# Performance work log

Hardware: AMD Instinct MI355X
Metric: run time of the kernel (lower is better)

## Reference

```python
import jax, jax.numpy as jnp
import numpy as np

E, HID, T, B, NH, DFF, A, C = 116, 64, 512, 64, 4, 2048, 116, 90


def _ln(x, g, b, eps=1e-5):
    m = x.mean(-1, keepdims=True)
    v = ((x - m) ** 2).mean(-1, keepdims=True)
    return (x - m) / jnp.sqrt(v + eps) * g + b


def _layer(x, p):
    # torch TransformerEncoderLayer, post-norm, relu, eval mode (no dropout)
    wqkv, bqkv, wo, bo, g1, bn1, w1, b1, w2, b2, g2, bn2 = p
    S, N, Em = x.shape  # note: S is the attended axis (dim 0), N the batched axis
    dh = Em // NH
    qkv = x @ wqkv.T + bqkv
    q, k, v = jnp.split(qkv, 3, axis=-1)
    q = q.reshape(S, N, NH, dh)
    k = k.reshape(S, N, NH, dh)
    v = v.reshape(S, N, NH, dh)
    scores = jnp.einsum('snhd,tnhd->nhst', q, k) / np.float32(np.sqrt(dh))
    attn = jax.nn.softmax(scores, axis=-1)
    o = jnp.einsum('nhst,tnhd->snhd', attn, v).reshape(S, N, Em)
    o = o @ wo.T + bo
    x = _ln(x + o, g1, bn1)
    f = jax.nn.relu(x @ w1.T + b1) @ w2.T + b2
    return _ln(x + f, g2, bn2)


def _forward(x, sim, p1, p2, fc_w, fc_b):
    out = _layer(x, p1)
    out1 = _layer(out, p2)
    outs = jnp.transpose(out1, (0, 2, 1))       # (B, E, T)
    fea_ = outs @ fc_w.T + fc_b                 # (B, E, HID)
    feas = jnp.transpose(fea_, (0, 2, 1))       # (B, HID, E)
    fea = feas[:, None, :, :, None]             # (B,1,HID,E,1)
    sim32 = sim.astype(jnp.float32)             # (A, HID, C)
    # cosine_similarity over the HID axis (dim=2 of broadcast tensors),
    # computed without materializing the (B,A,HID,E,C) broadcast product.
    dot = jnp.einsum('bhd,ahc->badc', feas, sim32)           # (B,A,E,C)
    fn = jnp.linalg.norm(feas, axis=1)                       # (B,E)
    sn = jnp.linalg.norm(sim32, axis=1)                      # (A,C)
    denom = jnp.maximum(fn[:, None, :, None] * sn[None, :, None, :], 1e-8)
    similarity = dot / denom                                 # (B,A,E,C)
    similar = similarity.reshape(-1, 116 * 90)
    nrm = jnp.maximum(jnp.linalg.norm(similar, axis=1, keepdims=True), 1e-12)
    similar = similar / nrm
    return fea, similarity, similar


_PNAMES = ['wqkv', 'bqkv', 'wo', 'bo', 'g1', 'bn1', 'w1', 'b1', 'w2', 'b2', 'g2', 'bn2']
_PSHAPES = [(3 * E, E), (3 * E,), (E, E), (E,), (E,), (E,), (DFF, E), (DFF,), (E, DFF), (E,), (E,), (E,)]


def setup_inputs() -> dict:
    key = jax.random.key(0)
    ks = jax.random.split(key, 32)
    s = 0.02
    inp = {
        'x': jax.random.normal(ks[0], (B, T, E), jnp.float32),
        'sim': jax.random.normal(ks[1], (A, HID, C), jnp.float32),
    }
    i = 2
    for L in ('l1', 'l2'):
        for nm, sh in zip(_PNAMES, _PSHAPES):
            if nm in ('g1', 'g2'):
                inp[f'{L}_{nm}'] = jnp.ones(sh, jnp.float32)
            elif nm in ('bqkv', 'bo', 'bn1', 'b1', 'b2', 'bn2'):
                inp[f'{L}_{nm}'] = jnp.zeros(sh, jnp.float32)
            else:
                inp[f'{L}_{nm}'] = jax.random.normal(ks[i], sh, jnp.float32) * s
                i += 1
    inp['fc_w'] = jax.random.normal(ks[i], (HID, T), jnp.float32) * s
    inp['fc_b'] = jnp.zeros((HID,), jnp.float32)
    return inp


def reference(x, sim,
              l1_wqkv, l1_bqkv, l1_wo, l1_bo, l1_g1, l1_bn1, l1_w1, l1_b1, l1_w2, l1_b2, l1_g2, l1_bn2,
              l2_wqkv, l2_bqkv, l2_wo, l2_bo, l2_g1, l2_bn1, l2_w1, l2_b1, l2_w2, l2_b2, l2_g2, l2_bn2,
              fc_w, fc_b):
    p1 = (l1_wqkv, l1_bqkv, l1_wo, l1_bo, l1_g1, l1_bn1, l1_w1, l1_b1, l1_w2, l1_b2, l1_g2, l1_bn2)
    p2 = (l2_wqkv, l2_bqkv, l2_wo, l2_bo, l2_g1, l2_bn1, l2_w1, l2_b1, l2_w2, l2_b2, l2_g2, l2_bn2)
    return _forward(x, sim, p1, p2, fc_w, fc_b)
```

## Files before the change

kernel.cpp:

```cpp
#include <hip/hip_runtime.h>
#include <hip/hip_bf16.h>

typedef __attribute__((ext_vector_type(8))) short short8v;
typedef __attribute__((ext_vector_type(4))) float floatx4;

__device__ __forceinline__ float bf2f(unsigned short u) {
  union { unsigned int i; float f; } c;
  c.i = ((unsigned int)u) << 16;
  return c.f;
}
__device__ __forceinline__ unsigned short f2bf(float f) {
  __hip_bfloat16 h = __float2bfloat16(f);
  return *reinterpret_cast<unsigned short*>(&h);
}

struct ConvJobs {
  const float* src[9];
  unsigned short* dst[9];
  int K[9];
  int Kp[9];
  int mode[9];
  int cum[10];
};

__global__ __launch_bounds__(256) void convert_all_kernel(ConvJobs J) {
  const int total = J.cum[9];
  for (int idx = blockIdx.x * 256 + threadIdx.x; idx < total;
       idx += gridDim.x * 256) {
    int j = 0;
    while (idx >= J.cum[j + 1]) ++j;
    const int local = idx - J.cum[j];
    const int Kp = J.Kp[j];
    const int r = local / Kp, c = local - r * Kp;
    unsigned short v;
    if (J.mode[j] == 0) {
      v = (c < J.K[j]) ? f2bf(J.src[j][(size_t)r * J.K[j] + c])
                       : (unsigned short)0;
    } else {
      const int h = c >> 5, d = c & 31;
      v = (d < 29) ? f2bf(J.src[j][(size_t)r * 116 + h * 29 + d])
                   : (unsigned short)0;
    }
    J.dst[j][local] = v;
  }
}

template <int MODE>
__global__ __launch_bounds__(256) void mgemm_kernel(
    const unsigned short* __restrict__ A, const unsigned short* __restrict__ B,
    const float* __restrict__ bias, int N, int Kp, int ldout,
    unsigned short* __restrict__ Yb) {
  __shared__ __align__(16) unsigned short As[128][64];
  __shared__ __align__(16) unsigned short Bs[128][64];

  const int tid = threadIdx.x;
  const int M0 = blockIdx.x * 128;
  const int N0 = blockIdx.y * 128;
  const int wid = tid >> 6, lane = tid & 63;
  const int wr = wid >> 1, wc = wid & 1;
  const int lc = lane & 15, g = lane >> 4;
  const int srow = tid >> 1, shalf = tid & 1;
  const int sw = srow & 7;

  floatx4 acc[4][4] = {};

  const int nk = Kp >> 6;
  for (int kt = 0; kt < nk; ++kt) {
    const int k0 = kt << 6;
    {
      const uint4* p = reinterpret_cast<const uint4*>(
          A + (size_t)(M0 + srow) * Kp + k0 + shalf * 32);
      uint4 v0 = p[0], v1 = p[1], v2 = p[2], v3 = p[3];
      *reinterpret_cast<uint4*>(&As[srow][((((shalf << 2) | 0) ^ sw) << 3)]) = v0;
      *reinterpret_cast<uint4*>(&As[srow][((((shalf << 2) | 1) ^ sw) << 3)]) = v1;
      *reinterpret_cast<uint4*>(&As[srow][((((shalf << 2) | 2) ^ sw) << 3)]) = v2;
      *reinterpret_cast<uint4*>(&As[srow][((((shalf << 2) | 3) ^ sw) << 3)]) = v3;
    }
    {
      uint4 v0 = {0, 0, 0, 0}, v1 = v0, v2 = v0, v3 = v0;
      const int jr = N0 + srow;
      if (jr < N) {
        const uint4* p = reinterpret_cast<const uint4*>(
            B + (size_t)jr * Kp + k0 + shalf * 32);
        v0 = p[0]; v1 = p[1]; v2 = p[2]; v3 = p[3];
      }
      *reinterpret_cast<uint4*>(&Bs[srow][((((shalf << 2) | 0) ^ sw) << 3)]) = v0;
      *reinterpret_cast<uint4*>(&Bs[srow][((((shalf << 2) | 1) ^ sw) << 3)]) = v1;
      *reinterpret_cast<uint4*>(&Bs[srow][((((shalf << 2) | 2) ^ sw) << 3)]) = v2;
      *reinterpret_cast<uint4*>(&Bs[srow][((((shalf << 2) | 3) ^ sw) << 3)]) = v3;
    }
    __syncthreads();
#pragma unroll
    for (int ks = 0; ks < 2; ++ks) {
      short8v a[4], b[4];
#pragma unroll
      for (int m = 0; m < 4; ++m) {
        const int row = wr * 64 + m * 16 + lc;
        a[m] = *reinterpret_cast<const short8v*>(
            &As[row][((((ks << 2) | g) ^ (lc & 7)) << 3)]);
      }
#pragma unroll
      for (int n = 0; n < 4; ++n) {
        const int col = wc * 64 + n * 16 + lc;
        b[n] = *reinterpret_cast<const short8v*>(
            &Bs[col][((((ks << 2) | g) ^ (lc & 7)) << 3)]);
      }
#pragma unroll
      for (int m = 0; m < 4; ++m)
#pragma unroll
        for (int n = 0; n < 4; ++n)
          acc[m][n] = __builtin_amdgcn_mfma_f32_16x16x32_bf16(a[m], b[n],
                                                              acc[m][n], 0, 0, 0);
    }
    __syncthreads();
  }

#pragma unroll
  for (int m = 0; m < 4; ++m) {
#pragma unroll
    for (int r = 0; r < 4; ++r) {
      const int row = M0 + wr * 64 + m * 16 + g * 4 + r;
#pragma unroll
      for (int n = 0; n < 4; ++n) {
        const int col = N0 + wc * 64 + n * 16 + lc;
        if (col < N) {
          float v = acc[m][n][r] + bias[col];
          if (MODE == 1) v = fmaxf(v, 0.f);
          if constexpr (MODE == 3) {
            const int which = (col >= 232) ? 2 : (col >= 116 ? 1 : 0);
            const int cw = col - which * 116;
            const int h = (cw * 565) >> 14;
            const int d = cw - h * 29;
            const int nn2 = row & 511, ss = row >> 9;
            Yb[(size_t)which * 4194304 +
               ((((size_t)nn2 * 4 + h) * 64 + ss) << 5) + d] = f2bf(v);
          } else {
            Yb[(size_t)row * ldout + col] = f2bf(v);
          }
        }
      }
    }
  }
}

__global__ __launch_bounds__(256) void mgemm64_ln_kernel(
    const unsigned short* __restrict__ A, const unsigned short* __restrict__ B,
    const float* __restrict__ bias, int Kp, unsigned short* __restrict__ Yb,
    float* __restrict__ Yf, const float* __restrict__ res,
    const float* __restrict__ gw, const float* __restrict__ bw) {
  __shared__ __align__(16) unsigned short As[64][64];
  __shared__ __align__(16) unsigned short Bs[128][64];
  __shared__ float sum1[2][64];
  __shared__ float sum2[2][64];

  const int tid = threadIdx.x;
  const int M0 = blockIdx.x * 64;
  const int wid = tid >> 6, lane = tid & 63;
  const int wr = wid >> 1, wc = wid & 1;
  const int lc = lane & 15, g = lane >> 4;
  const int arow = tid >> 2, aq = tid & 3;
  const int brow = tid >> 1, bhalf = tid & 1;

  floatx4 acc[2][4] = {};

  const int nk = Kp >> 6;
  for (int kt = 0; kt < nk; ++kt) {
    const int k0 = kt << 6;
    {
      const uint4* p = reinterpret_cast<const uint4*>(
          A + (size_t)(M0 + arow) * Kp + k0 + aq * 16);
      uint4 v0 = p[0], v1 = p[1];
      const int swa = arow & 7;
      *reinterpret_cast<uint4*>(&As[arow][(((aq * 2) ^ swa) << 3)]) = v0;
      *reinterpret_cast<uint4*>(&As[arow][(((aq * 2 + 1) ^ swa) << 3)]) = v1;
    }
    {
      uint4 v0 = {0, 0, 0, 0}, v1 = v0, v2 = v0, v3 = v0;
      if (brow < 116) {
        const uint4* p = reinterpret_cast<const uint4*>(
            B + (size_t)brow * Kp + k0 + bhalf * 32);
        v0 = p[0]; v1 = p[1]; v2 = p[2]; v3 = p[3];
      }
      const int sw = brow & 7;
      *reinterpret_cast<uint4*>(&Bs[brow][((((bhalf << 2) | 0) ^ sw) << 3)]) = v0;
      *reinterpret_cast<uint4*>(&Bs[brow][((((bhalf << 2) | 1) ^ sw) << 3)]) = v1;
      *reinterpret_cast<uint4*>(&Bs[brow][((((bhalf << 2) | 2) ^ sw) << 3)]) = v2;
      *reinterpret_cast<uint4*>(&Bs[brow][((((bhalf << 2) | 3) ^ sw) << 3)]) = v3;
    }
    __syncthreads();
#pragma unroll
    for (int ks = 0; ks < 2; ++ks) {
      short8v a[2], b[4];
#pragma unroll
      for (int m = 0; m < 2; ++m) {
        const int row = wr * 32 + m * 16 + lc;
        a[m] = *reinterpret_cast<const short8v*>(
            &As[row][((((ks << 2) | g) ^ (row & 7)) << 3)]);
      }
#pragma unroll
      for (int n = 0; n < 4; ++n) {
        const int col = wc * 64 + n * 16 + lc;
        b[n] = *reinterpret_cast<const short8v*>(
            &Bs[col][((((ks << 2) | g) ^ (col & 7)) << 3)]);
      }
#pragma unroll
      for (int m = 0; m < 2; ++m)
#pragma unroll
        for (int n = 0; n < 4; ++n)
          acc[m][n] = __builtin_amdgcn_mfma_f32_16x16x32_bf16(a[m], b[n],
                                                              acc[m][n], 0, 0, 0);
    }
    __syncthreads();
  }

  float s1l[2][4], s2l[2][4];
#pragma unroll
  for (int m = 0; m < 2; ++m) {
#pragma unroll
    for (int r = 0; r < 4; ++r) {
      const int row = M0 + wr * 32 + m * 16 + g * 4 + r;
      float s = 0.f, s2 = 0.f;
#pragma unroll
      for (int n = 0; n < 4; ++n) {
        const int col = wc * 64 + n * 16 + lc;
        float v = 0.f;
        if (col < 116)
          v = acc[m][n][r] + bias[col] + res[(size_t)row * 116 + col];
        acc[m][n][r] = v;
        s += v;
        s2 = fmaf(v, v, s2);
      }
#pragma unroll
      for (int st = 1; st < 16; st <<= 1) {
        s += __shfl_xor(s, st, 16);
        s2 += __shfl_xor(s2, st, 16);
      }
      s1l[m][r] = s;
      s2l[m][r] = s2;
    }
  }
  if (lc == 0) {
#pragma unroll
    for (int m = 0; m < 2; ++m)
#pragma unroll
      for (int r = 0; r < 4; ++r) {
        const int lrow = wr * 32 + m * 16 + g * 4 + r;
        sum1[wc][lrow] = s1l[m][r];
        sum2[wc][lrow] = s2l[m][r];
      }
  }
  __syncthreads();
#pragma unroll
  for (int m = 0; m < 2; ++m) {
#pragma unroll
    for (int r = 0; r < 4; ++r) {
      const int lrow = wr * 32 + m * 16 + g * 4 + r;
      const int row = M0 + lrow;
      const float st = sum1[0][lrow] + sum1[1][lrow];
      const float s2t = sum2[0][lrow] + sum2[1][lrow];
      const float mean = st * (1.f / 116.f);
      const float var = s2t * (1.f / 116.f) - mean * mean;
      const float rstd = 1.f / sqrtf(var + 1e-5f);
#pragma unroll
      for (int n = 0; n < 4; ++n) {
        const int col = wc * 64 + n * 16 + lc;
        if (col < 116) {
          const float y = (acc[m][n][r] - mean) * rstd * gw[col] + bw[col];
          Yf[(size_t)row * 116 + col] = y;
          Yb[(size_t)row * 128 + col] = f2bf(y);
        } else {
          Yb[(size_t)row * 128 + col] = 0;
        }
      }
    }
  }
}

__global__ __launch_bounds__(256) void ffn_fused_kernel(
    const unsigned short* __restrict__ Xa,
    const unsigned short* __restrict__ W1,
    const float* __restrict__ b1,
    const unsigned short* __restrict__ W2,
    const float* __restrict__ b2, const float* __restrict__ res,
    const float* __restrict__ gw, const float* __restrict__ bw,
    unsigned short* __restrict__ Yb,
    float* __restrict__ Yf) {
  __shared__ __align__(16) unsigned short Xs[64][128];
  __shared__ __align__(16) unsigned short W1c[64][128];
  __shared__ __align__(16) unsigned short W2c[128][64];
  __shared__ __align__(16) unsigned short Hs[64][64];
  __shared__ float sum1[2][64];
  __shared__ float sum2[2][64];

  const int tid = threadIdx.x;
  const int M0 = blockIdx.x * 64;
  const int wid = tid >> 6, lane = tid & 63;
  const int wr = wid >> 1, wc = wid & 1;
  const int lc = lane & 15, g = lane >> 4;
  const int arow = tid >> 2, aq = tid & 3;
  const int brow = tid >> 1, bh = tid & 1;

  {
    const uint4* p = reinterpret_cast<const uint4*>(
        Xa + (size_t)(M0 + arow) * 128 + aq * 32);
#pragma unroll
    for (int q = 0; q < 4; ++q) {
      const int cj = aq * 4 + q;
      const int swz = (cj & 8) | ((cj ^ arow) & 7);
      *reinterpret_cast<uint4*>(&Xs[arow][swz * 8]) = p[q];
    }
  }

  floatx4 oacc[2][4] = {};

  for (int kc = 0; kc < 32; ++kc) {
    {
      const uint4* p = reinterpret_cast<const uint4*>(
          W1 + (size_t)(kc * 64 + arow) * 128 + aq * 32);
#pragma unroll
      for (int q = 0; q < 4; ++q) {
        const int cj = aq * 4 + q;
        const int swz = (cj & 8) | ((cj ^ arow) & 7);
        *reinterpret_cast<uint4*>(&W1c[arow][swz * 8]) = p[q];
      }
    }
    {
      uint4 v[4] = {};
      if (brow < 116) {
        const uint4* p = reinterpret_cast<const uint4*>(
            W2 + (size_t)brow * 2048 + kc * 64 + bh * 32);
        v[0] = p[0]; v[1] = p[1]; v[2] = p[2]; v[3] = p[3];
      }
#pragma unroll
      for (int q = 0; q < 4; ++q) {
        const int cj = bh * 4 + q;
        const int swz = (cj ^ brow) & 7;
        *reinterpret_cast<uint4*>(&W2c[brow][swz * 8]) = v[q];
      }
    }
    __syncthreads();

    floatx4 hacc[2][2] = {};
#pragma unroll
    for (int ks = 0; ks < 4; ++ks) {
      short8v av[2], bv[2];
#pragma unroll
      for (int m = 0; m < 2; ++m) {
        const int row = wr * 32 + m * 16 + lc;
        const int cj = ks * 4 + g;
        const int swz = (cj & 8) | ((cj ^ row) & 7);
        av[m] = *reinterpret_cast<const short8v*>(&Xs[row][swz * 8]);
      }
#pragma unroll
      for (int n = 0; n < 2; ++n) {
        const int row = wc * 32 + n * 16 + lc;
        const int cj = ks * 4 + g;
        const int swz = (cj & 8) | ((cj ^ row) & 7);
        bv[n] = *reinterpret_cast<const short8v*>(&W1c[row][swz * 8]);
      }
#pragma unroll
      for (int m = 0; m < 2; ++m)
#pragma unroll
        for (int n = 0; n < 2; ++n)
          hacc[m][n] = __builtin_amdgcn_mfma_f32_16x16x32_bf16(av[m], bv[n],
                                                               hacc[m][n], 0, 0, 0);
    }
#pragma unroll
    for (int n = 0; n < 2; ++n) {
      const int dff = wc * 32 + n * 16 + lc;
      const float bb = b1[kc * 64 + dff];
      const int cj = dff >> 3;
      const int dlo = dff & 7;
#pragma unroll
      for (int m = 0; m < 2; ++m) {
#pragma unroll
        for (int r = 0; r < 4; ++r) {
          const int tok = wr * 32 + m * 16 + g * 4 + r;
          const float hv = fmaxf(hacc[m][n][r] + bb, 0.f);
          Hs[tok][(((cj ^ tok) & 7) << 3) | dlo] = f2bf(hv);
        }
      }
    }
    __syncthreads();

#pragma unroll
    for (int ks = 0; ks < 2; ++ks) {
      short8v av[2], bv[4];
#pragma unroll
      for (int m = 0; m < 2; ++m) {
        const int row = wr * 32 + m * 16 + lc;
        const int cj = ks * 4 + g;
        av[m] = *reinterpret_cast<const short8v*>(
            &Hs[row][(((cj ^ row) & 7) << 3)]);
      }
#pragma unroll
      for (int n = 0; n < 4; ++n) {
        const int col = wc * 64 + n * 16 + lc;
        const int cj = ks * 4 + g;
        bv[n] = *reinterpret_cast<const short8v*>(
            &W2c[col][(((cj ^ col) & 7) << 3)]);
      }
#pragma unroll
      for (int m = 0; m < 2; ++m)
#pragma unroll
        for (int n = 0; n < 4; ++n)
          oacc[m][n] = __builtin_amdgcn_mfma_f32_16x16x32_bf16(av[m], bv[n],
                                                               oacc[m][n], 0, 0, 0);
    }
    __syncthreads();
  }

  float s1l[2][4], s2l[2][4];
#pragma unroll
  for (int m = 0; m < 2; ++m) {
#pragma unroll
    for (int r = 0; r < 4; ++r) {
      const int row = M0 + wr * 32 + m * 16 + g * 4 + r;
      float s = 0.f, s2 = 0.f;
#pragma unroll
      for (int n = 0; n < 4; ++n) {
        const int col = wc * 64 + n * 16 + lc;
        float v = 0.f;
        if (col < 116)
          v = oacc[m][n][r] + b2[col] + res[(size_t)row * 116 + col];
        oacc[m][n][r] = v;
        s += v;
        s2 = fmaf(v, v, s2);
      }
#pragma unroll
      for (int st = 1; st < 16; st <<= 1) {
        s += __shfl_xor(s, st, 16);
        s2 += __shfl_xor(s2, st, 16);
      }
      s1l[m][r] = s;
      s2l[m][r] = s2;
    }
  }
  if (lc == 0) {
#pragma unroll
    for (int m = 0; m < 2; ++m)
#pragma unroll
      for (int r = 0; r < 4; ++r) {
        const int lrow = wr * 32 + m * 16 + g * 4 + r;
        sum1[wc][lrow] = s1l[m][r];
        sum2[wc][lrow] = s2l[m][r];
      }
  }
  __syncthreads();
#pragma unroll
  for (int m = 0; m < 2; ++m) {
#pragma unroll
    for (int r = 0; r < 4; ++r) {
      const int lrow = wr * 32 + m * 16 + g * 4 + r;
      const int row = M0 + lrow;
      const float st = sum1[0][lrow] + sum1[1][lrow];
      const float s2t = sum2[0][lrow] + sum2[1][lrow];
      const float mean = st * (1.f / 116.f);
      const float var = s2t * (1.f / 116.f) - mean * mean;
      const float rstd = 1.f / sqrtf(var + 1e-5f);
#pragma unroll
      for (int n = 0; n < 4; ++n) {
        const int col = wc * 64 + n * 16 + lc;
        if (col < 116) {
          const float y = (oacc[m][n][r] - mean) * rstd * gw[col] + bw[col];
          Yf[(size_t)row * 116 + col] = y;
          Yb[(size_t)row * 128 + col] = f2bf(y);
        } else {
          Yb[(size_t)row * 128 + col] = 0;
        }
      }
    }
  }
}

__global__ __launch_bounds__(64) void attn_kernel(
    const unsigned short* __restrict__ qkvp, unsigned short* __restrict__ obuf) {
  const int h = blockIdx.x & 3;
  const int n = blockIdx.x >> 2;
  const int s = threadIdx.x;
  __shared__ float ks[64][36];
  __shared__ float vs[64][36];

  const size_t rb = (((size_t)n * 4 + h) * 64 + s) * 32;
  const uint4* qp = reinterpret_cast<const uint4*>(qkvp + rb);
  const uint4* kp = reinterpret_cast<const uint4*>(qkvp + 4194304 + rb);
  const uint4* vp = reinterpret_cast<const uint4*>(qkvp + 8388608 + rb);
  uint4 qv[4], kv4[4], vv4[4];
#pragma unroll
  for (int i = 0; i < 4; ++i) {
    qv[i] = qp[i];
    kv4[i] = kp[i];
    vv4[i] = vp[i];
  }
  float q[32], kf[32], vf[32];
#pragma unroll
  for (int i = 0; i < 4; ++i) {
    const unsigned* wq = reinterpret_cast<const unsigned*>(&qv[i]);
    const unsigned* wk = reinterpret_cast<const unsigned*>(&kv4[i]);
    const unsigned* wv = reinterpret_cast<const unsigned*>(&vv4[i]);
#pragma unroll
    for (int j = 0; j < 4; ++j) {
      union { unsigned u; float f; } lo, hi;
      const int d0 = i * 8 + 2 * j;
      lo.u = wq[j] << 16; hi.u = wq[j] & 0xffff0000u;
      q[d0] = lo.f; q[d0 + 1] = hi.f;
      lo.u = wk[j] << 16; hi.u = wk[j] & 0xffff0000u;
      kf[d0] = (d0 < 29) ? lo.f : 0.f;
      kf[d0 + 1] = (d0 + 1 < 29) ? hi.f : 0.f;
      lo.u = wv[j] << 16; hi.u = wv[j] & 0xffff0000u;
      vf[d0] = (d0 < 29) ? lo.f : 0.f;
      vf[d0 + 1] = (d0 + 1 < 29) ? hi.f : 0.f;
    }
  }
  q[29] = q[30] = q[31] = 0.f;
#pragma unroll
  for (int c = 0; c < 8; ++c) {
    *reinterpret_cast<float4*>(&ks[s][c * 4]) =
        make_float4(kf[4 * c], kf[4 * c + 1], kf[4 * c + 2], kf[4 * c + 3]);
    *reinterpret_cast<float4*>(&vs[s][c * 4]) =
        make_float4(vf[4 * c], vf[4 * c + 1], vf[4 * c + 2], vf[4 * c + 3]);
  }
  __syncthreads();

  const float scale = 0.18569533817705186f;
  float sc[64];
#pragma unroll 4
  for (int t = 0; t < 64; ++t) {
    const float4* kr = reinterpret_cast<const float4*>(&ks[t][0]);
    float a = 0.f;
#pragma unroll
    for (int c = 0; c < 8; ++c) {
      const float4 kc = kr[c];
      a = fmaf(q[4 * c], kc.x, a);
      a = fmaf(q[4 * c + 1], kc.y, a);
      a = fmaf(q[4 * c + 2], kc.z, a);
      a = fmaf(q[4 * c + 3], kc.w, a);
    }
    sc[t] = a * scale;
  }
  float m = sc[0];
#pragma unroll
  for (int t = 1; t < 64; ++t) m = fmaxf(m, sc[t]);
  float sum = 0.f;
#pragma unroll
  for (int t = 0; t < 64; ++t) {
    sc[t] = __expf(sc[t] - m);
    sum += sc[t];
  }
  const float inv = 1.f / sum;
  float o[32] = {};
#pragma unroll 4
  for (int t = 0; t < 64; ++t) {
    const float p = sc[t];
    const float4* vr = reinterpret_cast<const float4*>(&vs[t][0]);
#pragma unroll
    for (int c = 0; c < 8; ++c) {
      const float4 vc = vr[c];
      o[4 * c] = fmaf(p, vc.x, o[4 * c]);
      o[4 * c + 1] = fmaf(p, vc.y, o[4 * c + 1]);
      o[4 * c + 2] = fmaf(p, vc.z, o[4 * c + 2]);
      o[4 * c + 3] = fmaf(p, vc.w, o[4 * c + 3]);
    }
  }
  unsigned short ow[32];
#pragma unroll
  for (int i = 0; i < 32; ++i) ow[i] = f2bf(o[i] * inv);
  uint4* od =
      reinterpret_cast<uint4*>(obuf + ((size_t)s * 512 + n) * 128 + h * 32);
  const uint4* ows = reinterpret_cast<const uint4*>(ow);
#pragma unroll
  for (int i = 0; i < 4; ++i) od[i] = ows[i];
}

__global__ __launch_bounds__(256) void fc_kernel(const float* __restrict__ X4,
                                                 const float* __restrict__ fw,
                                                 const float* __restrict__ fb,
                                                 float* __restrict__ fea) {
  const int eg = blockIdx.x;
  const int b = blockIdx.y;
  const int e0 = eg * 29;
  __shared__ float Os[64][30];
  __shared__ float Wf[64][65];
  const int tid = threadIdx.x;
  const int h = tid & 63, jg = tid >> 6;
  float acc[8] = {};

  for (int tc = 0; tc < 8; ++tc) {
    for (int idx = tid; idx < 64 * 29; idx += 256) {
      int tt = idx / 29;
      int ee = idx - tt * 29;
      Os[tt][ee] = X4[((size_t)b * 512 + tc * 64 + tt) * 116 + e0 + ee];
    }
    for (int idx = tid; idx < 64 * 64; idx += 256) {
      int hh = idx >> 6, t2 = idx & 63;
      Wf[hh][t2] = fw[(size_t)hh * 512 + tc * 64 + t2];
    }
    __syncthreads();
#pragma unroll 4
    for (int t = 0; t < 64; ++t) {
      const float w = Wf[h][t];
#pragma unroll
      for (int m = 0; m < 8; ++m) {
        const int el = jg + 4 * m;
        if (el < 29) acc[m] = fmaf(Os[t][el], w, acc[m]);
      }
    }
    __syncthreads();
  }
  const float bb = fb[h];
#pragma unroll
  for (int m = 0; m < 8; ++m) {
    const int el = jg + 4 * m;
    if (el < 29) fea[((size_t)b * 64 + h) * 116 + e0 + el] = acc[m] + bb;
  }
}

__global__ __launch_bounds__(256) void sim_prep_kernel(
    const float* __restrict__ fea, const float* __restrict__ simin,
    unsigned short* __restrict__ feaT, unsigned short* __restrict__ simT,
    float* __restrict__ fn, float* __restrict__ sn) {
  __shared__ float L[64][121];
  const int blk = blockIdx.x;
  const int tid = threadIdx.x;
  if (blk < 64) {
    const int b = blk;
    for (int idx = tid; idx < 64 * 116; idx += 256) {
      const int h = idx / 116, d = idx - h * 116;
      L[h][d] = bf2f(f2bf(fea[((size_t)b * 64 + h) * 116 + d]));
    }
    __syncthreads();
    for (int idx = tid; idx < 128 * 64; idx += 256) {
      const int d = idx >> 6, h = idx & 63;
      feaT[((size_t)b * 128 + d) * 64 + h] = (d < 116) ? f2bf(L[h][d]) : 0;
    }
    if (tid < 116) {
      float s = 0.f;
#pragma unroll 8
      for (int h = 0; h < 64; ++h) {
        const float t = L[h][tid];
        s = fmaf(t, t, s);
      }
      fn[b * 128 + tid] = sqrtf(s);
    }
  } else {
    const int a = blk - 64;
    for (int idx = tid; idx < 64 * 90; idx += 256) {
      const int h = idx / 90, c = idx - h * 90;
      L[h][c] = bf2f(f2bf(simin[((size_t)a * 64 + h) * 90 + c]));
    }
    __syncthreads();
    for (int idx = tid; idx < 96 * 64; idx += 256) {
      const int c = idx >> 6, h = idx & 63;
      simT[((size_t)a * 96 + c) * 64 + h] = (c < 90) ? f2bf(L[h][c]) : 0;
    }
    if (tid < 90) {
      float s = 0.f;
#pragma unroll 8
      for (int h = 0; h < 64; ++h) {
        const float t = L[h][tid];
        s = fmaf(t, t, s);
      }
      sn[a * 96 + tid] = sqrtf(s);
    }
  }
}

__global__ __launch_bounds__(256) void sim_mfma2_kernel(
    const unsigned short* __restrict__ feaT, const unsigned short* __restrict__ simT,
    const float* __restrict__ fn, const float* __restrict__ sn,
    float* __restrict__ simil, float* __restrict__ similar) {
  const int a = blockIdx.x;
  const int b = blockIdx.y;
  __shared__ __align__(16) unsigned char shmem[41760];
  __shared__ float fnrow[116];
  __shared__ float snrow[90];
  __shared__ float wred[4];
  const int tid = threadIdx.x;

  unsigned short (*Ft)[64] = reinterpret_cast<unsigned short(*)[64]>(shmem);
  unsigned short (*St)[64] =
      reinterpret_cast<unsigned short(*)[64]>(shmem + 16384);
  float* Rs = reinterpret_cast<float*>(shmem);

  const int srow = tid >> 1, shalf = tid & 1;
  const int sw = srow & 7;
  {
    const uint4* p = reinterpret_cast<const uint4*>(
        feaT + ((size_t)b * 128 + srow) * 64 + shalf * 32);
    uint4 v0 = p[0], v1 = p[1], v2 = p[2], v3 = p[3];
    *reinterpret_cast<uint4*>(&Ft[srow][((((shalf << 2) | 0) ^ sw) << 3)]) = v0;
    *reinterpret_cast<uint4*>(&Ft[srow][((((shalf << 2) | 1) ^ sw) << 3)]) = v1;
    *reinterpret_cast<uint4*>(&Ft[srow][((((shalf << 2) | 2) ^ sw) << 3)]) = v2;
    *reinterpret_cast<uint4*>(&Ft[srow][((((shalf << 2) | 3) ^ sw) << 3)]) = v3;
  }
  if (srow < 96) {
    const uint4* p = reinterpret_cast<const uint4*>(
        simT + ((size_t)a * 96 + srow) * 64 + shalf * 32);
    uint4 v0 = p[0], v1 = p[1], v2 = p[2], v3 = p[3];
    *reinterpret_cast<uint4*>(&St[srow][((((shalf << 2) | 0) ^ sw) << 3)]) = v0;
    *reinterpret_cast<uint4*>(&St[srow][((((shalf << 2) | 1) ^ sw) << 3)]) = v1;
    *reinterpret_cast<uint4*>(&St[srow][((((shalf << 2) | 2) ^ sw) << 3)]) = v2;
    *reinterpret_cast<uint4*>(&St[srow][((((shalf << 2) | 3) ^ sw) << 3)]) = v3;
  }
  if (tid < 116) fnrow[tid] = fn[b * 128 + tid];
  else if (tid >= 128 && tid < 218) snrow[tid - 128] = sn[a * 96 + tid - 128];
  __syncthreads();

  const int wid = tid >> 6, lane = tid & 63;
  const int wr = wid >> 1, wc = wid & 1;
  const int lc = lane & 15, g = lane >> 4;

  floatx4 acc[4][3] = {};
#pragma unroll
  for (int ks = 0; ks < 2; ++ks) {
    short8v av[4], bv[3];
#pragma unroll
    for (int m = 0; m < 4; ++m) {
      const int row = wr * 64 + m * 16 + lc;
      av[m] = *reinterpret_cast<const short8v*>(
          &Ft[row][((((ks << 2) | g) ^ (lc & 7)) << 3)]);
    }
#pragma unroll
    for (int n = 0; n < 3; ++n) {
      const int col = wc * 48 + n * 16 + lc;
      bv[n] = *reinterpret_cast<const short8v*>(
          &St[col][((((ks << 2) | g) ^ (lc & 7)) << 3)]);
    }
#pragma unroll
    for (int m = 0; m < 4; ++m)
#pragma unroll
      for (int n = 0; n < 3; ++n)
        acc[m][n] = __builtin_amdgcn_mfma_f32_16x16x32_bf16(av[m], bv[n],
                                                            acc[m][n], 0, 0, 0);
  }
  __syncthreads();

  float ss = 0.f;
#pragma unroll
  for (int m = 0; m < 4; ++m) {
#pragma unroll
    for (int r = 0; r < 4; ++r) {
      const int d = wr * 64 + m * 16 + g * 4 + r;
      if (d < 116) {
        const float fnv = fnrow[d];
#pragma unroll
        for (int n = 0; n < 3; ++n) {
          const int c = wc * 48 + n * 16 + lc;
          if (c < 90) {
            const float denom = fmaxf(fnv * snrow[c], 1e-8f);
            float rcp = __builtin_amdgcn_rcpf(denom);
            rcp = rcp * (2.0f - denom * rcp);
            const float v = acc[m][n][r] * rcp;
            ss = fmaf(v, v, ss);
            Rs[d * 90 + c] = v;
          }
        }
      }
    }
  }
#pragma unroll
  for (int st = 1; st <= 32; st <<= 1) ss += __shfl_xor(ss, st, 64);
  if (lane == 0) wred[wid] = ss;
  __syncthreads();
  const float tot = wred[0] + wred[1] + wred[2] + wred[3];
  const float inv = 1.f / fmaxf(sqrtf(tot), 1e-12f);

  const size_t rowbase = ((size_t)b * 116 + a) * (116 * 90);
  float4* so = reinterpret_cast<float4*>(simil + rowbase);
  float4* sr = reinterpret_cast<float4*>(similar + rowbase);
  const float4* rs4 = reinterpret_cast<const float4*>(Rs);
  for (int i = tid; i < 2610; i += 256) {
    float4 v = rs4[i];
    so[i] = v;
    float4 w;
    w.x = v.x * inv; w.y = v.y * inv; w.z = v.z * inv; w.w = v.w * inv;
    sr[i] = w;
  }
}

__global__ __launch_bounds__(256) void sim_mfma_kernel(
    const float* __restrict__ fea, const float* __restrict__ simin,
    float* __restrict__ simil, float* __restrict__ similar) {
  const int a = blockIdx.x;
  const int b = blockIdx.y;
  __shared__ __align__(16) unsigned char shmem[41760];
  __shared__ float fnrow[116];
  __shared__ float snrow[90];
  __shared__ float wred[4];
  const int tid = threadIdx.x;

  unsigned short (*Ft)[64] = reinterpret_cast<unsigned short(*)[64]>(shmem);
  unsigned short (*St)[64] =
      reinterpret_cast<unsigned short(*)[64]>(shmem + 16384);
  float* Rs = reinterpret_cast<float*>(shmem);

  for (int idx = tid; idx < 64 * 116; idx += 256) {
    const int h = idx / 116, d = idx - h * 116;
    Ft[d][(((h >> 3) ^ (d & 7)) << 3) | (h & 7)] =
        f2bf(fea[((size_t)b * 64 + h) * 116 + d]);
  }
  for (int idx = tid; idx < 12 * 64; idx += 256) {
    const int d = 116 + (idx >> 6), h = idx & 63;
    Ft[d][(((h >> 3) ^ (d & 7)) << 3) | (h & 7)] = 0;
  }
  for (int idx = tid; idx < 64 * 90; idx += 256) {
    const int h = idx / 90, c = idx - h * 90;
    St[c][(((h >> 3) ^ (c & 7)) << 3) | (h & 7)] =
        f2bf(simin[((size_t)a * 64 + h) * 90 + c]);
  }
  for (int idx = tid; idx < 6 * 64; idx += 256) {
    const int c = 90 + (idx >> 6), h = idx & 63;
    St[c][(((h >> 3) ^ (c & 7)) << 3) | (h & 7)] = 0;
  }
  __syncthreads();

  if (tid < 116) {
    float s = 0.f;
#pragma unroll 8
    for (int h = 0; h < 64; ++h) {
      const float t = bf2f(Ft[tid][(((h >> 3) ^ (tid & 7)) << 3) | (h & 7)]);
      s = fmaf(t, t, s);
    }
    fnrow[tid] = sqrtf(s);
  } else if (tid >= 128 && tid < 218) {
    const int c = tid - 128;
    float s = 0.f;
#pragma unroll 8
    for (int h = 0; h < 64; ++h) {
      const float t = bf2f(St[c][(((h >> 3) ^ (c & 7)) << 3) | (h & 7)]);
      s = fmaf(t, t, s);
    }
    snrow[c] = sqrtf(s);
  }
  __syncthreads();

  const int wid = tid >> 6, lane = tid & 63;
  const int wr = wid >> 1, wc = wid & 1;
  const int lc = lane & 15, g = lane >> 4;

  floatx4 acc[4][3] = {};
#pragma unroll
  for (int ks = 0; ks < 2; ++ks) {
    short8v av[4], bv[3];
#pragma unroll
    for (int m = 0; m < 4; ++m) {
      const int row = wr * 64 + m * 16 + lc;
      av[m] = *reinterpret_cast<const short8v*>(
          &Ft[row][((((ks << 2) | g) ^ (lc & 7)) << 3)]);
    }
#pragma unroll
    for (int n = 0; n < 3; ++n) {
      const int col = wc * 48 + n * 16 + lc;
      bv[n] = *reinterpret_cast<const short8v*>(
          &St[col][((((ks << 2) | g) ^ (lc & 7)) << 3)]);
    }
#pragma unroll
    for (int m = 0; m < 4; ++m)
#pragma unroll
      for (int n = 0; n < 3; ++n)
        acc[m][n] = __builtin_amdgcn_mfma_f32_16x16x32_bf16(av[m], bv[n],
                                                            acc[m][n], 0, 0, 0);
  }
  __syncthreads();

  float ss = 0.f;
#pragma unroll
  for (int m = 0; m < 4; ++m) {
#pragma unroll
    for (int r = 0; r < 4; ++r) {
      const int d = wr * 64 + m * 16 + g * 4 + r;
      if (d < 116) {
        const float fnv = fnrow[d];
#pragma unroll
        for (int n = 0; n < 3; ++n) {
          const int c = wc * 48 + n * 16 + lc;
          if (c < 90) {
            const float denom = fmaxf(fnv * snrow[c], 1e-8f);
            float rcp = __builtin_amdgcn_rcpf(denom);
            rcp = rcp * (2.0f - denom * rcp);
            const float v = acc[m][n][r] * rcp;
            ss = fmaf(v, v, ss);
            Rs[d * 90 + c] = v;
          }
        }
      }
    }
  }
#pragma unroll
  for (int st = 1; st <= 32; st <<= 1) ss += __shfl_xor(ss, st, 64);
  if (lane == 0) wred[wid] = ss;
  __syncthreads();
  const float tot = wred[0] + wred[1] + wred[2] + wred[3];
  const float inv = 1.f / fmaxf(sqrtf(tot), 1e-12f);

  const size_t rowbase = ((size_t)b * 116 + a) * (116 * 90);
  float4* so = reinterpret_cast<float4*>(simil + rowbase);
  float4* sr = reinterpret_cast<float4*>(similar + rowbase);
  const float4* rs4 = reinterpret_cast<const float4*>(Rs);
  for (int i = tid; i < 2610; i += 256) {
    float4 v = rs4[i];
    so[i] = v;
    float4 w;
    w.x = v.x * inv; w.y = v.y * inv; w.z = v.z * inv; w.w = v.w * inv;
    sr[i] = w;
  }
}

extern "C" void kernel_launch(void* const* d_in, const int* in_sizes, int n_in,
                              void* d_out, int out_size, void* d_ws,
                              size_t ws_size, hipStream_t stream) {
  const float* x0 = (const float*)d_in[0];
  const float* simin = (const float*)d_in[1];
  const float* p[24];
  for (int i = 0; i < 24; ++i) p[i] = (const float*)d_in[2 + i];
  const float* fc_w = (const float*)d_in[26];
  const float* fc_b = (const float*)d_in[27];

  float* out = (float*)d_out;
  float* fea = out;
  float* simil = out + 475136;
  float* similar = out + 77981696;

  float* xa_f[2] = {similar + 0, similar + 7602176};
  float* xb_f[2] = {similar + 3801088, similar + 11403264};
  unsigned short* obufb = (unsigned short*)(similar + 15204352);
  unsigned short* qkvp = (unsigned short*)(similar + 17301504);
  unsigned short* Ab = (unsigned short*)(similar + 23592960);
  unsigned short* xab[2] = {(unsigned short*)(similar + 25690112),
                            (unsigned short*)(similar + 29884416)};
  unsigned short* xbb[2] = {(unsigned short*)(similar + 27787264),
                            (unsigned short*)(similar + 31981568)};
  unsigned short* wbuf = (unsigned short*)(simil + 33554432);
  const size_t WSZ = 559104;

  unsigned char* ws = (unsigned char*)d_ws;
  unsigned short* feaT = (unsigned short*)ws;
  unsigned short* simT = (unsigned short*)(ws + 1048576);
  float* fnb = (float*)(ws + 2473984);
  float* snb = (float*)(ws + 2506752);
  const bool ws_ok = ws_size >= 2551296;

  {
    ConvJobs J;
    int cum = 0;
    auto add = [&](int j, const float* s, unsigned short* dd, int R, int K,
                   int Kp, int mode) {
      J.src[j] = s; J.dst[j] = dd; J.K[j] = K; J.Kp[j] = Kp; J.mode[j] = mode;
      J.cum[j] = cum; cum += R * Kp;
    };
    add(0, x0, Ab, 32768, 116, 128, 0);
    for (int L = 0; L < 2; ++L) {
      unsigned short* wb = wbuf + L * WSZ;
      add(1 + L * 4, p[L * 12 + 0], wb + 0, 348, 116, 128, 0);
      add(2 + L * 4, p[L * 12 + 2], wb + 44544, 116, 116, 128, 1);
      add(3 + L * 4, p[L * 12 + 6], wb + 59392, 2048, 116, 128, 0);
      add(4 + L * 4, p[L * 12 + 8], wb + 321536, 116, 2048, 2048, 0);
    }
    J.cum[9] = cum;
    hipLaunchKernelGGL(convert_all_kernel, dim3(2048), dim3(256), 0, stream, J);
  }

  const unsigned short* Ain = Ab;
  const float* resin = x0;
  for (int L = 0; L < 2; ++L) {
    unsigned short* wb = wbuf + L * WSZ;
    const float* bqkv = p[L * 12 + 1];
    const float* bo = p[L * 12 + 3];
    const float* g1 = p[L * 12 + 4];
    const float* bn1 = p[L * 12 + 5];
    const float* b1 = p[L * 12 + 7];
    const float* b2 = p[L * 12 + 9];
    const float* g2 = p[L * 12 + 10];
    const float* bn2 = p[L * 12 + 11];

    hipLaunchKernelGGL((mgemm_kernel<3>), dim3(256, 3), dim3(256), 0, stream,
                       Ain, wb + 0, bqkv, 348, 128, 0, qkvp);
    hipLaunchKernelGGL(attn_kernel, dim3(2048), dim3(64), 0, stream, qkvp,
                       obufb);
    hipLaunchKernelGGL(mgemm64_ln_kernel, dim3(512), dim3(256), 0, stream,
                       obufb, wb + 44544, bo, 128, xab[L], xa_f[L], resin, g1,
                       bn1);
    hipLaunchKernelGGL(ffn_fused_kernel, dim3(512), dim3(256), 0, stream,
                       xab[L], wb + 59392, b1, wb + 321536, b2, xa_f[L], g2,
                       bn2, xbb[L], xb_f[L]);
    Ain = xbb[L];
    resin = xb_f[L];
  }

  hipLaunchKernelGGL(fc_kernel, dim3(4, 64), dim3(256), 0, stream, xb_f[1],
                     fc_w, fc_b, fea);
  if (ws_ok) {
    hipLaunchKernelGGL(sim_prep_kernel, dim3(180), dim3(256), 0, stream, fea,
                       simin, feaT, simT, fnb, snb);
    hipLaunchKernelGGL(sim_mfma2_kernel, dim3(116, 64), dim3(256), 0, stream,
                       feaT, simT, fnb, snb, simil, similar);
  } else {
    hipLaunchKernelGGL(sim_mfma_kernel, dim3(116, 64), dim3(256), 0, stream,
                       fea, simin, simil, similar);
  }
}
```

Measured before the change: 662.8 us.

## Prefetch FFN weights in registers, fuse fea transpose into fc, batch sim blocks

The FFN kernel now loads the next W1/W2 chunk into registers while the current chunk is being consumed, which overlaps global loads with compute. The fc kernel now also writes the bf16 transposed features and their norms directly, using a wave shuffle reduction, so the fea half of sim_prep is removed. The sim-table prep moves earlier into its own kernel. The similarity kernel now handles 4 values of a per block, reusing the loaded feature tile. One risk: the padding rows of feaT are no longer zeroed, but the outputs that would use them are discarded anyway.

```diff
diff --git a/kernel.cpp b/kernel.cpp
--- a/kernel.cpp
+++ b/kernel.cpp
@@ -311,31 +311,47 @@
     }
   }
 
+  uint4 w1r[4], w2r[4];
+  {
+    const uint4* p1 =
+        reinterpret_cast<const uint4*>(W1 + (size_t)arow * 128 + aq * 32);
+#pragma unroll
+    for (int q = 0; q < 4; ++q) w1r[q] = p1[q];
+    uint4 z = {0, 0, 0, 0};
+    w2r[0] = z; w2r[1] = z; w2r[2] = z; w2r[3] = z;
+    if (brow < 116) {
+      const uint4* p2 =
+          reinterpret_cast<const uint4*>(W2 + (size_t)brow * 2048 + bh * 32);
+#pragma unroll
+      for (int q = 0; q < 4; ++q) w2r[q] = p2[q];
+    }
+  }
+
   floatx4 oacc[2][4] = {};
 
   for (int kc = 0; kc < 32; ++kc) {
-    {
-      const uint4* p = reinterpret_cast<const uint4*>(
-          W1 + (size_t)(kc * 64 + arow) * 128 + aq * 32);
-#pragma unroll
-      for (int q = 0; q < 4; ++q) {
-        const int cj = aq * 4 + q;
-        const int swz = (cj & 8) | ((cj ^ arow) & 7);
-        *reinterpret_cast<uint4*>(&W1c[arow][swz * 8]) = p[q];
-      }
-    }
-    {
-      uint4 v[4] = {};
+#pragma unroll
+    for (int q = 0; q < 4; ++q) {
+      const int cj = aq * 4 + q;
+      const int swz = (cj & 8) | ((cj ^ arow) & 7);
+      *reinterpret_cast<uint4*>(&W1c[arow][swz * 8]) = w1r[q];
+    }
+#pragma unroll
+    for (int q = 0; q < 4; ++q) {
+      const int cj = bh * 4 + q;
+      const int swz = (cj ^ brow) & 7;
+      *reinterpret_cast<uint4*>(&W2c[brow][swz * 8]) = w2r[q];
+    }
+    if (kc < 31) {
+      const uint4* p1 = reinterpret_cast<const uint4*>(
+          W1 + (size_t)((kc + 1) * 64 + arow) * 128 + aq * 32);
+#pragma unroll
+      for (int q = 0; q < 4; ++q) w1r[q] = p1[q];
       if (brow < 116) {
-        const uint4* p = reinterpret_cast<const uint4*>(
-            W2 + (size_t)brow * 2048 + kc * 64 + bh * 32);
-        v[0] = p[0]; v[1] = p[1]; v[2] = p[2]; v[3] = p[3];
-      }
-#pragma unroll
-      for (int q = 0; q < 4; ++q) {
-        const int cj = bh * 4 + q;
-        const int swz = (cj ^ brow) & 7;
-        *reinterpret_cast<uint4*>(&W2c[brow][swz * 8]) = v[q];
+        const uint4* p2 = reinterpret_cast<const uint4*>(
+            W2 + (size_t)brow * 2048 + (kc + 1) * 64 + bh * 32);
+#pragma unroll
+        for (int q = 0; q < 4; ++q) w2r[q] = p2[q];
       }
     }
     __syncthreads();
@@ -572,10 +588,10 @@
   for (int i = 0; i < 4; ++i) od[i] = ows[i];
 }
 
-__global__ __launch_bounds__(256) void fc_kernel(const float* __restrict__ X4,
-                                                 const float* __restrict__ fw,
-                                                 const float* __restrict__ fb,
-                                                 float* __restrict__ fea) {
+__global__ __launch_bounds__(256) void fc_kernel(
+    const float* __restrict__ X4, const float* __restrict__ fw,
+    const float* __restrict__ fb, float* __restrict__ fea,
+    unsigned short* __restrict__ feaT, float* __restrict__ fn) {
   const int eg = blockIdx.x;
   const int b = blockIdx.y;
   const int e0 = eg * 29;
@@ -611,79 +627,68 @@
 #pragma unroll
   for (int m = 0; m < 8; ++m) {
     const int el = jg + 4 * m;
-    if (el < 29) fea[((size_t)b * 64 + h) * 116 + e0 + el] = acc[m] + bb;
-  }
-}
-
-__global__ __launch_bounds__(256) void sim_prep_kernel(
-    const float* __restrict__ fea, const float* __restrict__ simin,
-    unsigned short* __restrict__ feaT, unsigned short* __restrict__ simT,
-    float* __restrict__ fn, float* __restrict__ sn) {
-  __shared__ float L[64][121];
-  const int blk = blockIdx.x;
+    if (el < 29) {
+      const float v = acc[m] + bb;
+      const int e = e0 + el;
+      fea[((size_t)b * 64 + h) * 116 + e] = v;
+      if (feaT) {
+        const unsigned short vb = f2bf(v);
+        feaT[((size_t)b * 128 + e) * 64 + h] = vb;
+        float s = bf2f(vb);
+        s = s * s;
+#pragma unroll
+        for (int st = 1; st <= 32; st <<= 1) s += __shfl_xor(s, st, 64);
+        if (h == 0) fn[b * 128 + e] = sqrtf(s);
+      }
+    }
+  }
+}
+
+__global__ __launch_bounds__(256) void simt_prep_kernel(
+    const float* __restrict__ simin, unsigned short* __restrict__ simT,
+    float* __restrict__ sn) {
+  __shared__ float L[64][91];
+  const int a = blockIdx.x;
   const int tid = threadIdx.x;
-  if (blk < 64) {
-    const int b = blk;
-    for (int idx = tid; idx < 64 * 116; idx += 256) {
-      const int h = idx / 116, d = idx - h * 116;
-      L[h][d] = bf2f(f2bf(fea[((size_t)b * 64 + h) * 116 + d]));
-    }
-    __syncthreads();
-    for (int idx = tid; idx < 128 * 64; idx += 256) {
-      const int d = idx >> 6, h = idx & 63;
-      feaT[((size_t)b * 128 + d) * 64 + h] = (d < 116) ? f2bf(L[h][d]) : 0;
-    }
-    if (tid < 116) {
-      float s = 0.f;
+  for (int idx = tid; idx < 64 * 90; idx += 256) {
+    const int h = idx / 90, c = idx - h * 90;
+    L[h][c] = bf2f(f2bf(simin[((size_t)a * 64 + h) * 90 + c]));
+  }
+  __syncthreads();
+  for (int idx = tid; idx < 96 * 64; idx += 256) {
+    const int c = idx >> 6, h = idx & 63;
+    simT[((size_t)a * 96 + c) * 64 + h] = (c < 90) ? f2bf(L[h][c]) : 0;
+  }
+  if (tid < 90) {
+    float s = 0.f;
 #pragma unroll 8
-      for (int h = 0; h < 64; ++h) {
-        const float t = L[h][tid];
-        s = fmaf(t, t, s);
-      }
-      fn[b * 128 + tid] = sqrtf(s);
-    }
-  } else {
-    const int a = blk - 64;
-    for (int idx = tid; idx < 64 * 90; idx += 256) {
-      const int h = idx / 90, c = idx - h * 90;
-      L[h][c] = bf2f(f2bf(simin[((size_t)a * 64 + h) * 90 + c]));
-    }
-    __syncthreads();
-    for (int idx = tid; idx < 96 * 64; idx += 256) {
-      const int c = idx >> 6, h = idx & 63;
-      simT[((size_t)a * 96 + c) * 64 + h] = (c < 90) ? f2bf(L[h][c]) : 0;
-    }
-    if (tid < 90) {
-      float s = 0.f;
-#pragma unroll 8
-      for (int h = 0; h < 64; ++h) {
-        const float t = L[h][tid];
-        s = fmaf(t, t, s);
-      }
-      sn[a * 96 + tid] = sqrtf(s);
-    }
-  }
-}
-
-__global__ __launch_bounds__(256) void sim_mfma2_kernel(
+    for (int h = 0; h < 64; ++h) {
+      const float t = L[h][tid];
+      s = fmaf(t, t, s);
+    }
+    sn[a * 96 + tid] = sqrtf(s);
+  }
+}
+
+__global__ __launch_bounds__(256) void sim_mfma3_kernel(
     const unsigned short* __restrict__ feaT, const unsigned short* __restrict__ simT,
     const float* __restrict__ fn, const float* __restrict__ sn,
     float* __restrict__ simil, float* __restrict__ similar) {
-  const int a = blockIdx.x;
+  const int a0 = blockIdx.x * 4;
   const int b = blockIdx.y;
-  __shared__ __align__(16) unsigned char shmem[41760];
+  __shared__ __align__(16) unsigned short Ft[128][64];
+  __shared__ __align__(16) unsigned short St[96][64];
+  __shared__ __align__(16) float Rs[10440];
   __shared__ float fnrow[116];
   __shared__ float snrow[90];
   __shared__ float wred[4];
   const int tid = threadIdx.x;
-
-  unsigned short (*Ft)[64] = reinterpret_cast<unsigned short(*)[64]>(shmem);
-  unsigned short (*St)[64] =
-      reinterpret_cast<unsigned short(*)[64]>(shmem + 16384);
-  float* Rs = reinterpret_cast<float*>(shmem);
-
   const int srow = tid >> 1, shalf = tid & 1;
   const int sw = srow & 7;
+  const int wid = tid >> 6, lane = tid & 63;
+  const int wr = wid >> 1, wc = wid & 1;
+  const int lc = lane & 15, g = lane >> 4;
+
   {
     const uint4* p = reinterpret_cast<const uint4*>(
         feaT + ((size_t)b * 128 + srow) * 64 + shalf * 32);
@@ -693,88 +698,87 @@
     *reinterpret_cast<uint4*>(&Ft[srow][((((shalf << 2) | 2) ^ sw) << 3)]) = v2;
     *reinterpret_cast<uint4*>(&Ft[srow][((((shalf << 2) | 3) ^ sw) << 3)]) = v3;
   }
-  if (srow < 96) {
-    const uint4* p = reinterpret_cast<const uint4*>(
-        simT + ((size_t)a * 96 + srow) * 64 + shalf * 32);
-    uint4 v0 = p[0], v1 = p[1], v2 = p[2], v3 = p[3];
-    *reinterpret_cast<uint4*>(&St[srow][((((shalf << 2) | 0) ^ sw) << 3)]) = v0;
-    *reinterpret_cast<uint4*>(&St[srow][((((shalf << 2) | 1) ^ sw) << 3)]) = v1;
-    *reinterpret_cast<uint4*>(&St[srow][((((shalf << 2) | 2) ^ sw) << 3)]) = v2;
-    *reinterpret_cast<uint4*>(&St[srow][((((shalf << 2) | 3) ^ sw) << 3)]) = v3;
-  }
   if (tid < 116) fnrow[tid] = fn[b * 128 + tid];
-  else if (tid >= 128 && tid < 218) snrow[tid - 128] = sn[a * 96 + tid - 128];
-  __syncthreads();
-
-  const int wid = tid >> 6, lane = tid & 63;
-  const int wr = wid >> 1, wc = wid & 1;
-  const int lc = lane & 15, g = lane >> 4;
-
-  floatx4 acc[4][3] = {};
-#pragma unroll
-  for (int ks = 0; ks < 2; ++ks) {
-    short8v av[4], bv[3];
+
+  for (int ai = 0; ai < 4; ++ai) {
+    const int a = a0 + ai;
+    if (srow < 96) {
+      const uint4* p = reinterpret_cast<const uint4*>(
+          simT + ((size_t)a * 96 + srow) * 64 + shalf * 32);
+      uint4 v0 = p[0], v1 = p[1], v2 = p[2], v3 = p[3];
+      *reinterpret_cast<uint4*>(&St[srow][((((shalf << 2) | 0) ^ sw) << 3)]) = v0;
+      *reinterpret_cast<uint4*>(&St[srow][((((shalf << 2) | 1) ^ sw) << 3)]) = v1;
+      *reinterpret_cast<uint4*>(&St[srow][((((shalf << 2) | 2) ^ sw) << 3)]) = v2;
+      *reinterpret_cast<uint4*>(&St[srow][((((shalf << 2) | 3) ^ sw) << 3)]) = v3;
+    }
+    if (tid >= 160 && tid < 250) snrow[tid - 160] = sn[a * 96 + (tid - 160)];
+    __syncthreads();
+
+    floatx4 acc[4][3] = {};
+#pragma unroll
+    for (int ks = 0; ks < 2; ++ks) {
+      short8v av[4], bv[3];
+#pragma unroll
+      for (int m = 0; m < 4; ++m) {
+        const int row = wr * 64 + m * 16 + lc;
+        av[m] = *reinterpret_cast<const short8v*>(
+            &Ft[row][((((ks << 2) | g) ^ (lc & 7)) << 3)]);
+      }
+#pragma unroll
+      for (int n = 0; n < 3; ++n) {
+        const int col = wc * 48 + n * 16 + lc;
+        bv[n] = *reinterpret_cast<const short8v*>(
+            &St[col][((((ks << 2) | g) ^ (lc & 7)) << 3)]);
+      }
+#pragma unroll
+      for (int m = 0; m < 4; ++m)
+#pragma unroll
+        for (int n = 0; n < 3; ++n)
+          acc[m][n] = __builtin_amdgcn_mfma_f32_16x16x32_bf16(av[m], bv[n],
+                                                              acc[m][n], 0, 0, 0);
+    }
+
+    float ss = 0.f;
 #pragma unroll
     for (int m = 0; m < 4; ++m) {
-      const int row = wr * 64 + m * 16 + lc;
-      av[m] = *reinterpret_cast<const short8v*>(
-          &Ft[row][((((ks << 2) | g) ^ (lc & 7)) << 3)]);
-    }
-#pragma unroll
-    for (int n = 0; n < 3; ++n) {
-      const int col = wc * 48 + n * 16 + lc;
-      bv[n] = *reinterpret_cast<const short8v*>(
-          &St[col][((((ks << 2) | g) ^ (lc & 7)) << 3)]);
-    }
-#pragma unroll
-    for (int m = 0; m < 4; ++m)
-#pragma unroll
-      for (int n = 0; n < 3; ++n)
-        acc[m][n] = __builtin_amdgcn_mfma_f32_16x16x32_bf16(av[m], bv[n],
-                                                            acc[m][n], 0, 0, 0);
-  }
-  __syncthreads();
-
-  float ss = 0.f;
-#pragma unroll
-  for (int m = 0; m < 4; ++m) {
-#pragma unroll
-    for (int r = 0; r < 4; ++r) {
-      const int d = wr * 64 + m * 16 + g * 4 + r;
-      if (d < 116) {
-        const float fnv = fnrow[d];
-#pragma unroll
-        for (int n = 0; n < 3; ++n) {
-          const int c = wc * 48 + n * 16 + lc;
-          if (c < 90) {
-            const float denom = fmaxf(fnv * snrow[c], 1e-8f);
-            float rcp = __builtin_amdgcn_rcpf(denom);
-            rcp = rcp * (2.0f - denom * rcp);
-            const float v = acc[m][n][r] * rcp;
-            ss = fmaf(v, v, ss);
-            Rs[d * 90 + c] = v;
+#pragma unroll
+      for (int r = 0; r < 4; ++r) {
+        const int d = wr * 64 + m * 16 + g * 4 + r;
+        if (d < 116) {
+          const float fnv = fnrow[d];
+#pragma unroll
+          for (int n = 0; n < 3; ++n) {
+            const int c = wc * 48 + n * 16 + lc;
+            if (c < 90) {
+              const float denom = fmaxf(fnv * snrow[c], 1e-8f);
+              float rcp = __builtin_amdgcn_rcpf(denom);
+              rcp = rcp * (2.0f - denom * rcp);
+              const float v = acc[m][n][r] * rcp;
+              ss = fmaf(v, v, ss);
+              Rs[d * 90 + c] = v;
+            }
           }
         }
       }
     }
-  }
-#pragma unroll
-  for (int st = 1; st <= 32; st <<= 1) ss += __shfl_xor(ss, st, 64);
-  if (lane == 0) wred[wid] = ss;
-  __syncthreads();
-  const float tot = wred[0] + wred[1] + wred[2] + wred[3];
-  const float inv = 1.f / fmaxf(sqrtf(tot), 1e-12f);
-
-  const size_t rowbase = ((size_t)b * 116 + a) * (116 * 90);
-  float4* so = reinterpret_cast<float4*>(simil + rowbase);
-  float4* sr = reinterpret_cast<float4*>(similar + rowbase);
-  const float4* rs4 = reinterpret_cast<const float4*>(Rs);
-  for (int i = tid; i < 2610; i += 256) {
-    float4 v = rs4[i];
-    so[i] = v;
-    float4 w;
-    w.x = v.x * inv; w.y = v.y * inv; w.z = v.z * inv; w.w = v.w * inv;
-    sr[i] = w;
+#pragma unroll
+    for (int st = 1; st <= 32; st <<= 1) ss += __shfl_xor(ss, st, 64);
+    if (lane == 0) wred[wid] = ss;
+    __syncthreads();
+    const float tot = wred[0] + wred[1] + wred[2] + wred[3];
+    const float inv = 1.f / fmaxf(sqrtf(tot), 1e-12f);
+
+    const size_t rowbase = ((size_t)b * 116 + a) * (116 * 90);
+    float4* so = reinterpret_cast<float4*>(simil + rowbase);
+    float4* sr = reinterpret_cast<float4*>(similar + rowbase);
+    const float4* rs4 = reinterpret_cast<const float4*>(Rs);
+    for (int i = tid; i < 2610; i += 256) {
+      float4 v = rs4[i];
+      so[i] = v;
+      float4 w;
+      w.x = v.x * inv; w.y = v.y * inv; w.z = v.z * inv; w.w = v.w * inv;
+      sr[i] = w;
+    }
   }
 }
 
@@ -960,6 +964,11 @@
     hipLaunchKernelGGL(convert_all_kernel, dim3(2048), dim3(256), 0, stream, J);
   }
 
+  if (ws_ok) {
+    hipLaunchKernelGGL(simt_prep_kernel, dim3(116), dim3(256), 0, stream,
+                       simin, simT, snb);
+  }
+
   const unsigned short* Ain = Ab;
   const float* resin = x0;
   for (int L = 0; L < 2; ++L) {
@@ -987,14 +996,15 @@
     resin = xb_f[L];
   }
 
-  hipLaunchKernelGGL(fc_kernel, dim3(4, 64), dim3(256), 0, stream, xb_f[1],
-                     fc_w, fc_b, fea);
   if (ws_ok) {
-    hipLaunchKernelGGL(sim_prep_kernel, dim3(180), dim3(256), 0, stream, fea,
-                       simin, feaT, simT, fnb, snb);
-    hipLaunchKernelGGL(sim_mfma2_kernel, dim3(116, 64), dim3(256), 0, stream,
+    hipLaunchKernelGGL(fc_kernel, dim3(4, 64), dim3(256), 0, stream, xb_f[1],
+                       fc_w, fc_b, fea, feaT, fnb);
+    hipLaunchKernelGGL(sim_mfma3_kernel, dim3(29, 64), dim3(256), 0, stream,
                        feaT, simT, fnb, snb, simil, similar);
   } else {
+    hipLaunchKernelGGL(fc_kernel, dim3(4, 64), dim3(256), 0, stream, xb_f[1],
+                       fc_w, fc_b, fea, (unsigned short*)nullptr,
+                       (float*)nullptr);
     hipLaunchKernelGGL(sim_mfma_kernel, dim3(116, 64), dim3(256), 0, stream,
                        fea, simin, simil, similar);
   }
```

New measurement: 664.5 us. Within noise of the previous version (+0.2%).
